# Performance work log

Hardware: AMD Instinct MI355X
Metric: run time of the kernel (lower is better)

## Reference

```python
import jax, jax.numpy as jnp
import numpy as np

BATCH, IN_DIM, OUT_DIM, G, K = 8192, 256, 64, 64, 4
T0, T1 = 0.0, 1.0


def _bspline_basis(x, t, k):
    """Cox-de Boor recursion, vectorized over all basis indices.

    x: [B, D] evaluation points; t: [T] knot vector (non-decreasing).
    Returns basis values of order k: [B, D, T-k].
    """
    xb = x[..., None]  # [B, D, 1]
    # order-1 (degree-0) bases: indicator of half-open knot interval
    b = ((xb >= t[:-1]) & (xb < t[1:])).astype(x.dtype)  # [B, D, T-1]
    T = t.shape[0]
    for p in range(2, k + 1):
        n = T - p  # number of order-p bases
        d1 = t[p - 1:p - 1 + n] - t[:n]          # left denominators
        d2 = t[p:p + n] - t[1:1 + n]             # right denominators
        w1 = jnp.where(d1 > 0, (xb - t[:n]) / jnp.where(d1 > 0, d1, 1.0), 0.0)
        w2 = jnp.where(d2 > 0, (t[p:p + n] - xb) / jnp.where(d2 > 0, d2, 1.0), 0.0)
        b = w1 * b[..., :n] + w2 * b[..., 1:n + 1]
    return b  # [B, D, T-k]


def setup_inputs() -> dict:
    key = jax.random.key(0)
    kx, kw = jax.random.split(key)
    x = jax.random.uniform(kx, (BATCH, IN_DIM), dtype=jnp.float32)
    fan_in = (G + K) * IN_DIM
    std = float(np.sqrt(2.0 / (fan_in + OUT_DIM)))  # xavier_normal_
    w = jax.random.normal(kw, (fan_in, OUT_DIM), dtype=jnp.float32) * std
    inner = jnp.linspace(T0, T1, G + 1, dtype=jnp.float32)
    t = jnp.concatenate([jnp.full((K - 1,), T0, jnp.float32), inner,
                         jnp.full((K - 1,), T1, jnp.float32)], 0)  # [G+2k-1]
    return {"x": x, "w": w, "t": t, "k": K}


def reference(x, w, t, k):
    y1 = _bspline_basis(x, t, k)                       # [B, D, G+k-1]
    y2 = jnp.concatenate([y1, jax.nn.silu(x)[..., None]], axis=2)  # [B, D, G+k]
    return y2.reshape(x.shape[0], -1) @ w              # [B, out_dim]
```

## Files before the change

### kernel.cpp

```cpp
#include <hip/hip_runtime.h>
#include <stdint.h>

#define BATCH   8192
#define IN_DIM  256
#define OUT_DIM 64
#define NROW    68
#define N_SPLIT 16
#define D_SLICE 16
#define D_STAGE 2
#define N_STAGE 8
#define M_BLK   256
#define NM      32

typedef unsigned int u32;
typedef float f32x4 __attribute__((ext_vector_type(4)));
typedef __bf16 bf16x2 __attribute__((ext_vector_type(2)));

#if defined(__has_builtin)
#  if __has_builtin(__builtin_amdgcn_fdot2_f32_bf16)
#    define HAVE_DOT2 1
#  endif
#endif
#ifndef HAVE_DOT2
#  define HAVE_DOT2 0
#endif

__device__ __forceinline__ u32 f2bf(float f) {
    u32 u = __float_as_uint(f);
    u += 0x7FFFu + ((u >> 16) & 1u);
    return u >> 16;
}
__device__ __forceinline__ float bflo(u32 u) { return __uint_as_float(u << 16); }
__device__ __forceinline__ float bfhi(u32 u) { return __uint_as_float(u & 0xFFFF0000u); }

__device__ __forceinline__ u32 pkbf(float lo, float hi) {
    bf16x2 v = { (__bf16)lo, (__bf16)hi };
    u32 u;
    __builtin_memcpy(&u, &v, 4);
    return u;
}

__device__ __forceinline__ float dot2bf(u32 a, u32 b, float c) {
#if HAVE_DOT2
    bf16x2 av, bv;
    __builtin_memcpy(&av, &a, 4);
    __builtin_memcpy(&bv, &b, 4);
    return __builtin_amdgcn_fdot2_f32_bf16(av, bv, c, false);
#else
    return fmaf(bflo(a), bflo(b), fmaf(bfhi(a), bfhi(b), c));
#endif
}

__device__ __forceinline__ float knotf(int i) {
    return fminf(1.f, fmaxf(0.f, (float)(i - 3) * 0.015625f));
}

__device__ __forceinline__ void make_record(float x, u32 rec[4]) {
    int s = (int)floorf(x * 64.f);
    s = max(0, min(63, s));
    const int m = s + 3;
    float N0 = 1.f, N1, N2, N3;
    const float l1 = x - knotf(m);
    const float r1 = knotf(m + 1) - x;
    {
        float tmp = N0 / (r1 + l1);
        N0 = r1 * tmp;
        N1 = l1 * tmp;
    }
    const float l2 = x - knotf(m - 1);
    const float r2 = knotf(m + 2) - x;
    {
        float tmp = N0 / (r1 + l2);
        N0 = r1 * tmp;
        float saved = l2 * tmp;
        tmp = N1 / (r2 + l1);
        N1 = saved + r2 * tmp;
        N2 = l1 * tmp;
    }
    const float l3 = x - knotf(m - 2);
    const float r3 = knotf(m + 3) - x;
    {
        float tmp = N0 / (r1 + l3);
        N0 = r1 * tmp;
        float saved = l3 * tmp;
        tmp = N1 / (r2 + l2);
        N1 = saved + r2 * tmp;
        saved = l2 * tmp;
        tmp = N2 / (r3 + l1);
        N2 = saved + r3 * tmp;
        N3 = l1 * tmp;
    }
    const float silu = x / (1.f + __expf(-x));
    rec[0] = f2bf(N0) | (f2bf(N1) << 16);
    rec[1] = f2bf(N2) | (f2bf(N3) << 16);
    rec[2] = __float_as_uint(silu);
    rec[3] = (u32)s;
}

#define TAB_D     16896
#define SILU_OFF  33792
#define REC_OFF   34048
#define LDS_U4    2640

__global__ __launch_bounds__(512, 3)
void kan_main(const float* __restrict__ X, const float* __restrict__ W,
              float* __restrict__ outbuf, int useAtomic) {
    __shared__ uint4 smem4[LDS_U4];
    char* sm = (char*)smem4;

    const int mb  = blockIdx.x;
    const int sp  = blockIdx.y;
    const int tid = threadIdx.x;
    const int r0  = mb * M_BLK;
    const int d0  = sp * D_SLICE;

    const int lane = tid & 63;
    const int wv   = tid >> 6;
    const int sub  = lane & 7;
    const int g    = lane >> 3;
    const int rb   = wv * 32;

    float acc[4][8];
#pragma unroll
    for (int t = 0; t < 4; ++t)
#pragma unroll
        for (int k = 0; k < 8; ++k) acc[t][k] = 0.f;

    for (int st = 0; st < N_STAGE; ++st) {
        const int ds = d0 + st * D_STAGE;
        __syncthreads();

        {
            const float* wbase = W + (size_t)ds * (NROW * OUT_DIM);
            for (int i = tid; i < 2 * 66 * 16; i += 512) {
                const int dl  = (i >= 1056) ? 1 : 0;
                const int rem = i - dl * 1056;
                const int r   = rem >> 4;
                const int c16 = rem & 15;
                const float* p = wbase + (size_t)dl * (NROW * OUT_DIM)
                               + r * OUT_DIM + (c16 << 2);
                float4 va = *(const float4*)p;
                float4 vb = *(const float4*)(p + OUT_DIM);
                const int byte = dl * TAB_D + r * 256
                               + (((c16 >> 1) ^ (r & 7)) << 5) + ((c16 & 1) << 4);
                *(uint4*)(sm + byte) = make_uint4(pkbf(va.x, vb.x), pkbf(va.y, vb.y),
                                                  pkbf(va.z, vb.z), pkbf(va.w, vb.w));
            }
            if (tid >= 448) {
                int j = tid - 448;
                const int dl = j >> 5; j &= 31;
                const float* p = wbase + (size_t)dl * (NROW * OUT_DIM)
                               + 67 * OUT_DIM + j * 2;
                *(u32*)(sm + SILU_OFF + dl * 128 + j * 4) = pkbf(p[0], p[1]);
            }
        }
        {
            const int r  = tid & 255;
            const int dh = tid >> 8;
            const float x = X[(size_t)(r0 + r) * IN_DIM + ds + dh];
            u32 rec[4];
            make_record(x, rec);
            *(uint4*)(sm + REC_OFF + ((dh * 256 + r) << 4)) =
                make_uint4(rec[0], rec[1], rec[2], rec[3]);
        }
        __syncthreads();

#pragma unroll
        for (int dl = 0; dl < D_STAGE; ++dl) {
            const int tb = dl * TAB_D;
            uint4 wp = *(const uint4*)(sm + SILU_OFF + dl * 128 + sub * 16);
            float w67f[8];
            w67f[0] = bflo(wp.x); w67f[1] = bfhi(wp.x);
            w67f[2] = bflo(wp.y); w67f[3] = bfhi(wp.y);
            w67f[4] = bflo(wp.z); w67f[5] = bfhi(wp.z);
            w67f[6] = bflo(wp.w); w67f[7] = bfhi(wp.w);
#pragma unroll
            for (int t = 0; t < 4; ++t) {
                const uint4 rec = *(const uint4*)(sm + REC_OFF +
                                                  ((dl * 256 + rb + t * 8 + g) << 4));
                const u32 c01 = rec.x, c23 = rec.y;
                const float silu = __uint_as_float(rec.z);
                const int s = (int)rec.w;
                const char* a1 = sm + tb + s * 256 + (((sub ^ s) & 7) << 5);
                const char* a2 = sm + tb + (s + 2) * 256 + (((sub ^ (s + 2)) & 7) << 5);
                const uint4 p1  = *(const uint4*)(a1);
                const uint4 p1b = *(const uint4*)(a1 + 16);
                const uint4 p2  = *(const uint4*)(a2);
                const uint4 p2b = *(const uint4*)(a2 + 16);
                acc[t][0] = dot2bf(c23, p2.x,  dot2bf(c01, p1.x,  acc[t][0]));
                acc[t][1] = dot2bf(c23, p2.y,  dot2bf(c01, p1.y,  acc[t][1]));
                acc[t][2] = dot2bf(c23, p2.z,  dot2bf(c01, p1.z,  acc[t][2]));
                acc[t][3] = dot2bf(c23, p2.w,  dot2bf(c01, p1.w,  acc[t][3]));
                acc[t][4] = dot2bf(c23, p2b.x, dot2bf(c01, p1b.x, acc[t][4]));
                acc[t][5] = dot2bf(c23, p2b.y, dot2bf(c01, p1b.y, acc[t][5]));
                acc[t][6] = dot2bf(c23, p2b.z, dot2bf(c01, p1b.z, acc[t][6]));
                acc[t][7] = dot2bf(c23, p2b.w, dot2bf(c01, p1b.w, acc[t][7]));
#pragma unroll
                for (int k = 0; k < 8; ++k)
                    acc[t][k] = fmaf(silu, w67f[k], acc[t][k]);
            }
        }
    }

    if (!useAtomic) {
        float* wsp = outbuf + (size_t)sp * (BATCH * OUT_DIM);
#pragma unroll
        for (int t = 0; t < 4; ++t) {
            const int R = r0 + rb + t * 8 + g;
            f32x4 lo = { acc[t][0], acc[t][1], acc[t][2], acc[t][3] };
            f32x4 hi = { acc[t][4], acc[t][5], acc[t][6], acc[t][7] };
            __builtin_nontemporal_store(lo, (f32x4*)(wsp + (size_t)R * 64 + sub * 8));
            __builtin_nontemporal_store(hi, (f32x4*)(wsp + (size_t)R * 64 + sub * 8 + 4));
        }
    } else {
#pragma unroll
        for (int t = 0; t < 4; ++t) {
            const int R = r0 + rb + t * 8 + g;
#pragma unroll
            for (int k = 0; k < 8; ++k)
                atomicAdd(outbuf + (size_t)R * 64 + sub * 8 + k, acc[t][k]);
        }
    }
}

__global__ __launch_bounds__(256)
void kan_reduce(const float* __restrict__ ws, float* __restrict__ out) {
    const int i = blockIdx.x * 256 + threadIdx.x;
    const f32x4* w4 = (const f32x4*)ws;
    f32x4 a = __builtin_nontemporal_load(&w4[i]);
#pragma unroll
    for (int s = 1; s < N_SPLIT; ++s) {
        f32x4 b = __builtin_nontemporal_load(
            &w4[(size_t)s * (BATCH * OUT_DIM / 4) + i]);
        a += b;
    }
    *(f32x4*)((float*)out + (size_t)i * 4) = a;
}

extern "C" void kernel_launch(void* const* d_in, const int* in_sizes, int n_in,
                              void* d_out, int out_size, void* d_ws, size_t ws_size,
                              hipStream_t stream) {
    const float* X = (const float*)d_in[0];
    const float* W = (const float*)d_in[1];
    float* out = (float*)d_out;
    const size_t need = (size_t)N_SPLIT * BATCH * OUT_DIM * sizeof(float);
    dim3 grid(NM, N_SPLIT);
    if (ws_size >= need) {
        kan_main<<<grid, 512, 0, stream>>>(X, W, (float*)d_ws, 0);
        kan_reduce<<<(BATCH * OUT_DIM / 4) / 256, 256, 0, stream>>>((const float*)d_ws, out);
    } else {
        (void)hipMemsetAsync(d_out, 0, (size_t)out_size * sizeof(float), stream);
        kan_main<<<grid, 512, 0, stream>>>(X, W, out, 1);
    }
}
```

Measured before the change: 60.58 us.

## Store split-K partials as bf16 and drop LDS weight swizzle

Per-split partial sums are now packed to bf16 before they go to the workspace, which halves the bytes kan_main writes and kan_reduce reads. The reduce kernel unpacks the values and accumulates in fp32. The weight table in LDS drops the XOR swizzle for a linear layout in which each lane reads output columns sub*4 and 32+sub*4, so output columns are remapped. The silu weights are kept in fp32 instead of bf16. The bf16 partials lose precision, and the unswizzled layout may bring back LDS bank conflicts.

```diff
diff --git a/kernel.cpp b/kernel.cpp
--- a/kernel.cpp
+++ b/kernel.cpp
@@ -14,6 +14,7 @@
 
 typedef unsigned int u32;
 typedef float f32x4 __attribute__((ext_vector_type(4)));
+typedef u32   u32x2 __attribute__((ext_vector_type(2)));
 typedef __bf16 bf16x2 __attribute__((ext_vector_type(2)));
 
 #if defined(__has_builtin)
@@ -99,12 +100,12 @@
 
 #define TAB_D     16896
 #define SILU_OFF  33792
-#define REC_OFF   34048
-#define LDS_U4    2640
+#define REC_OFF   34304
+#define LDS_U4    2656
 
 __global__ __launch_bounds__(512, 3)
 void kan_main(const float* __restrict__ X, const float* __restrict__ W,
-              float* __restrict__ outbuf, int useAtomic) {
+              void* __restrict__ outbuf, int useAtomic) {
     __shared__ uint4 smem4[LDS_U4];
     char* sm = (char*)smem4;
 
@@ -141,17 +142,17 @@
                                + r * OUT_DIM + (c16 << 2);
                 float4 va = *(const float4*)p;
                 float4 vb = *(const float4*)(p + OUT_DIM);
-                const int byte = dl * TAB_D + r * 256
-                               + (((c16 >> 1) ^ (r & 7)) << 5) + ((c16 & 1) << 4);
+                const int byte = dl * TAB_D + r * 256 + (c16 << 4);
                 *(uint4*)(sm + byte) = make_uint4(pkbf(va.x, vb.x), pkbf(va.y, vb.y),
                                                   pkbf(va.z, vb.z), pkbf(va.w, vb.w));
             }
             if (tid >= 448) {
-                int j = tid - 448;
-                const int dl = j >> 5; j &= 31;
-                const float* p = wbase + (size_t)dl * (NROW * OUT_DIM)
-                               + 67 * OUT_DIM + j * 2;
-                *(u32*)(sm + SILU_OFF + dl * 128 + j * 4) = pkbf(p[0], p[1]);
+                const int j = tid - 448;
+#pragma unroll
+                for (int dl = 0; dl < 2; ++dl) {
+                    *(float*)(sm + SILU_OFF + dl * 256 + j * 4) =
+                        wbase[(size_t)dl * (NROW * OUT_DIM) + 67 * OUT_DIM + j];
+                }
             }
         }
         {
@@ -168,12 +169,8 @@
 #pragma unroll
         for (int dl = 0; dl < D_STAGE; ++dl) {
             const int tb = dl * TAB_D;
-            uint4 wp = *(const uint4*)(sm + SILU_OFF + dl * 128 + sub * 16);
-            float w67f[8];
-            w67f[0] = bflo(wp.x); w67f[1] = bfhi(wp.x);
-            w67f[2] = bflo(wp.y); w67f[3] = bfhi(wp.y);
-            w67f[4] = bflo(wp.z); w67f[5] = bfhi(wp.z);
-            w67f[6] = bflo(wp.w); w67f[7] = bfhi(wp.w);
+            const f32x4 w67a = *(const f32x4*)(sm + SILU_OFF + dl * 256 + sub * 16);
+            const f32x4 w67b = *(const f32x4*)(sm + SILU_OFF + dl * 256 + 128 + sub * 16);
 #pragma unroll
             for (int t = 0; t < 4; ++t) {
                 const uint4 rec = *(const uint4*)(sm + REC_OFF +
@@ -181,12 +178,12 @@
                 const u32 c01 = rec.x, c23 = rec.y;
                 const float silu = __uint_as_float(rec.z);
                 const int s = (int)rec.w;
-                const char* a1 = sm + tb + s * 256 + (((sub ^ s) & 7) << 5);
-                const char* a2 = sm + tb + (s + 2) * 256 + (((sub ^ (s + 2)) & 7) << 5);
-                const uint4 p1  = *(const uint4*)(a1);
-                const uint4 p1b = *(const uint4*)(a1 + 16);
-                const uint4 p2  = *(const uint4*)(a2);
-                const uint4 p2b = *(const uint4*)(a2 + 16);
+                const char* r1 = sm + tb + s * 256 + sub * 16;
+                const char* r2 = sm + tb + (s + 2) * 256 + sub * 16;
+                const uint4 p1  = *(const uint4*)(r1);
+                const uint4 p1b = *(const uint4*)(r1 + 128);
+                const uint4 p2  = *(const uint4*)(r2);
+                const uint4 p2b = *(const uint4*)(r2 + 128);
                 acc[t][0] = dot2bf(c23, p2.x,  dot2bf(c01, p1.x,  acc[t][0]));
                 acc[t][1] = dot2bf(c23, p2.y,  dot2bf(c01, p1.y,  acc[t][1]));
                 acc[t][2] = dot2bf(c23, p2.z,  dot2bf(c01, p1.z,  acc[t][2]));
@@ -195,46 +192,56 @@
                 acc[t][5] = dot2bf(c23, p2b.y, dot2bf(c01, p1b.y, acc[t][5]));
                 acc[t][6] = dot2bf(c23, p2b.z, dot2bf(c01, p1b.z, acc[t][6]));
                 acc[t][7] = dot2bf(c23, p2b.w, dot2bf(c01, p1b.w, acc[t][7]));
-#pragma unroll
-                for (int k = 0; k < 8; ++k)
-                    acc[t][k] = fmaf(silu, w67f[k], acc[t][k]);
+                acc[t][0] = fmaf(silu, w67a.x, acc[t][0]);
+                acc[t][1] = fmaf(silu, w67a.y, acc[t][1]);
+                acc[t][2] = fmaf(silu, w67a.z, acc[t][2]);
+                acc[t][3] = fmaf(silu, w67a.w, acc[t][3]);
+                acc[t][4] = fmaf(silu, w67b.x, acc[t][4]);
+                acc[t][5] = fmaf(silu, w67b.y, acc[t][5]);
+                acc[t][6] = fmaf(silu, w67b.z, acc[t][6]);
+                acc[t][7] = fmaf(silu, w67b.w, acc[t][7]);
             }
         }
     }
 
     if (!useAtomic) {
-        float* wsp = outbuf + (size_t)sp * (BATCH * OUT_DIM);
+        char* wsp = (char*)outbuf + (size_t)sp * (BATCH * OUT_DIM * 2);
 #pragma unroll
         for (int t = 0; t < 4; ++t) {
             const int R = r0 + rb + t * 8 + g;
-            f32x4 lo = { acc[t][0], acc[t][1], acc[t][2], acc[t][3] };
-            f32x4 hi = { acc[t][4], acc[t][5], acc[t][6], acc[t][7] };
-            __builtin_nontemporal_store(lo, (f32x4*)(wsp + (size_t)R * 64 + sub * 8));
-            __builtin_nontemporal_store(hi, (f32x4*)(wsp + (size_t)R * 64 + sub * 8 + 4));
+            u32x2 lo = { pkbf(acc[t][0], acc[t][1]), pkbf(acc[t][2], acc[t][3]) };
+            u32x2 hi = { pkbf(acc[t][4], acc[t][5]), pkbf(acc[t][6], acc[t][7]) };
+            __builtin_nontemporal_store(lo, (u32x2*)(wsp + (size_t)R * 128 + sub * 8));
+            __builtin_nontemporal_store(hi, (u32x2*)(wsp + (size_t)R * 128 + 64 + sub * 8));
         }
     } else {
+        float* out = (float*)outbuf;
 #pragma unroll
         for (int t = 0; t < 4; ++t) {
             const int R = r0 + rb + t * 8 + g;
 #pragma unroll
-            for (int k = 0; k < 8; ++k)
-                atomicAdd(outbuf + (size_t)R * 64 + sub * 8 + k, acc[t][k]);
+            for (int k = 0; k < 4; ++k) {
+                atomicAdd(out + (size_t)R * 64 + sub * 4 + k, acc[t][k]);
+                atomicAdd(out + (size_t)R * 64 + 32 + sub * 4 + k, acc[t][k + 4]);
+            }
         }
     }
 }
 
 __global__ __launch_bounds__(256)
-void kan_reduce(const float* __restrict__ ws, float* __restrict__ out) {
+void kan_reduce(const u32* __restrict__ ws, float* __restrict__ out) {
     const int i = blockIdx.x * 256 + threadIdx.x;
-    const f32x4* w4 = (const f32x4*)ws;
-    f32x4 a = __builtin_nontemporal_load(&w4[i]);
-#pragma unroll
-    for (int s = 1; s < N_SPLIT; ++s) {
-        f32x4 b = __builtin_nontemporal_load(
-            &w4[(size_t)s * (BATCH * OUT_DIM / 4) + i]);
-        a += b;
-    }
-    *(f32x4*)((float*)out + (size_t)i * 4) = a;
+    const u32x2* w2 = (const u32x2*)ws;
+    float a0 = 0.f, a1 = 0.f, a2 = 0.f, a3 = 0.f;
+#pragma unroll
+    for (int s = 0; s < N_SPLIT; ++s) {
+        u32x2 v = __builtin_nontemporal_load(
+            &w2[(size_t)s * (BATCH * OUT_DIM / 4) + i]);
+        a0 += bflo(v.x); a1 += bfhi(v.x);
+        a2 += bflo(v.y); a3 += bfhi(v.y);
+    }
+    f32x4 r = { a0, a1, a2, a3 };
+    *(f32x4*)(out + (size_t)i * 4) = r;
 }
 
 extern "C" void kernel_launch(void* const* d_in, const int* in_sizes, int n_in,
@@ -243,13 +250,13 @@
     const float* X = (const float*)d_in[0];
     const float* W = (const float*)d_in[1];
     float* out = (float*)d_out;
-    const size_t need = (size_t)N_SPLIT * BATCH * OUT_DIM * sizeof(float);
+    const size_t need = (size_t)N_SPLIT * BATCH * OUT_DIM * 2;
     dim3 grid(NM, N_SPLIT);
     if (ws_size >= need) {
-        kan_main<<<grid, 512, 0, stream>>>(X, W, (float*)d_ws, 0);
-        kan_reduce<<<(BATCH * OUT_DIM / 4) / 256, 256, 0, stream>>>((const float*)d_ws, out);
+        kan_main<<<grid, 512, 0, stream>>>(X, W, d_ws, 0);
+        kan_reduce<<<(BATCH * OUT_DIM / 4) / 256, 256, 0, stream>>>((const u32*)d_ws, out);
     } else {
         (void)hipMemsetAsync(d_out, 0, (size_t)out_size * sizeof(float), stream);
-        kan_main<<<grid, 512, 0, stream>>>(X, W, out, 1);
-    }
-}
+        kan_main<<<grid, 512, 0, stream>>>(X, W, d_out, 1);
+    }
+}
```

After: 49.20 us, median of 3. 18.8% less time.
